# Optimization experiments

Hardware: AMD Instinct MI355X
Metric: run time of the kernel (lower is better)

Reference implementation:

```python
import jax, jax.numpy as jnp
import numpy as np

N, K, D_IN, H = 8192, 8, 512, 512
SCALE = 0.02  # weight init scale


def setup_inputs() -> dict:
    key = jax.random.key(0)
    ks = jax.random.split(key, 12)
    inp = {
        "x": jax.random.normal(ks[0], (N, D_IN), jnp.float32),
        "child_h": jax.random.normal(ks[1], (N, K, H), jnp.float32),
        "child_c": jax.random.normal(ks[2], (N, K, H), jnp.float32),
    }
    names = ["i", "f", "o", "u"]
    for idx, g in enumerate(names):
        inp["W" + g] = jax.random.normal(ks[3 + idx], (D_IN, H), jnp.float32) * SCALE
        inp["bW" + g] = jnp.zeros((H,), jnp.float32)
        inp["U" + g] = jax.random.normal(ks[7 + idx], (H, H), jnp.float32) * SCALE
        inp["bU" + g] = jnp.zeros((H,), jnp.float32)
    return inp


def reference(x, child_h, child_c,
              Wi, bWi, Ui, bUi,
              Wf, bWf, Uf, bUf,
              Wo, bWo, Uo, bUo,
              Wu, bWu, Uu, bUu):
    # Child-Sum Tree-LSTM, batched over N nodes each with K children.
    h_sum = child_h.sum(axis=1)                                   # [N, H]
    i = jax.nn.sigmoid(x @ Wi + bWi + h_sum @ Ui + bUi)           # [N, H]
    o = jax.nn.sigmoid(x @ Wo + bWo + h_sum @ Uo + bUo)           # [N, H]
    u = jnp.tanh(x @ Wu + bWu + h_sum @ Uu + bUu)                 # [N, H]
    # Per-child forget gates: f_k = sigmoid(W_f x + U_f h_k)
    f = jax.nn.sigmoid((x @ Wf + bWf)[:, None, :]
                       + jnp.einsum('nkh,hg->nkg', child_h, Uf) + bUf)  # [N, K, H]
    c = i * u + (f * child_c).sum(axis=1)                         # [N, H]
    h = o * jnp.tanh(c)                                           # [N, H]
    return jnp.stack([h, c], axis=0)                              # [2, N, H]
```

## Files before the change

kernel.cpp:

```cpp
#include <hip/hip_runtime.h>
#include <hip/hip_bf16.h>


#define NN 8192
#define KCH 8
#define HH 512

typedef __attribute__((ext_vector_type(4))) float f32x4;
typedef __attribute__((ext_vector_type(8))) short short8;

__device__ inline unsigned short f2bf(float f) {
    union { float f; unsigned u; } v; v.f = f;
    unsigned r = v.u + 0x7FFFu + ((v.u >> 16) & 1u);
    return (unsigned short)(r >> 16);
}
__device__ inline float bf2f(unsigned short b) {
    union { unsigned u; float f; } v; v.u = ((unsigned)b) << 16;
    return v.f;
}
__device__ inline float sigm(float x) { return 1.f / (1.f + __expf(-x)); }
__device__ inline float tanh_pf(float x) { return 2.f / (1.f + __expf(-2.f * x)) - 1.f; }

__device__ __forceinline__ void gl16(const unsigned short* gsrc, unsigned short* ldst) {
    __builtin_amdgcn_global_load_lds(
        (const __attribute__((address_space(1))) unsigned int*)gsrc,
        (__attribute__((address_space(3))) unsigned int*)ldst,
        16, 0, 0);
}


__global__ void k_cvt(const float* __restrict__ in, unsigned short* __restrict__ outp) {
    int i = blockIdx.x * blockDim.x + threadIdx.x;
    float4 a = ((const float4*)in)[2 * i];
    float4 b = ((const float4*)in)[2 * i + 1];
    uint4 o;
    o.x = (unsigned)f2bf(a.x) | ((unsigned)f2bf(a.y) << 16);
    o.y = (unsigned)f2bf(a.z) | ((unsigned)f2bf(a.w) << 16);
    o.z = (unsigned)f2bf(b.x) | ((unsigned)f2bf(b.y) << 16);
    o.w = (unsigned)f2bf(b.z) | ((unsigned)f2bf(b.w) << 16);
    ((uint4*)outp)[i] = o;
}

__global__ void k_hsum(const float* __restrict__ ch, unsigned short* __restrict__ hs) {
    int i = blockIdx.x * blockDim.x + threadIdx.x;
    int n = i >> 7, h4 = i & 127;
    const float4* base = (const float4*)(ch + (size_t)n * KCH * HH) + h4;
    float4 s = base[0];
#pragma unroll
    for (int k = 1; k < KCH; ++k) {
        float4 v = base[(size_t)k * 128];
        s.x += v.x; s.y += v.y; s.z += v.z; s.w += v.w;
    }
    unsigned long long pk = (unsigned long long)f2bf(s.x)
        | ((unsigned long long)f2bf(s.y) << 16)
        | ((unsigned long long)f2bf(s.z) << 32)
        | ((unsigned long long)f2bf(s.w) << 48);
    *(unsigned long long*)&hs[(size_t)i * 4] = pk;
}

struct P8 { const float* p[8]; };
__global__ void k_transpose_w(P8 wsrc, unsigned short* __restrict__ out) {
    __shared__ float tile[32][33];
    const float* W = wsrc.p[blockIdx.z];
    unsigned short* O = out + (size_t)blockIdx.z * 262144;
    int k0 = blockIdx.x * 32, c0 = blockIdx.y * 32;
    for (int r = threadIdx.y; r < 32; r += 8)
        tile[r][threadIdx.x] = W[(size_t)(k0 + r) * 512 + c0 + threadIdx.x];
    __syncthreads();
    for (int r = threadIdx.y; r < 32; r += 8)
        O[(size_t)(c0 + r) * 512 + k0 + threadIdx.x] = f2bf(tile[threadIdx.x][r]);
}

__device__ __forceinline__ void gate_mfma(f32x4 (&acc)[4][2], const short8 (&af)[4],
                                          const unsigned short (*bl)[32], int bcol, int koff) {
    short8 b0 = *(const short8*)&bl[bcol][koff];
    short8 b1 = *(const short8*)&bl[bcol + 16][koff];
#pragma unroll
    for (int m = 0; m < 4; ++m) {
        acc[m][0] = __builtin_amdgcn_mfma_f32_16x16x32_bf16(af[m], b0, acc[m][0], 0, 0, 0);
        acc[m][1] = __builtin_amdgcn_mfma_f32_16x16x32_bf16(af[m], b1, acc[m][1], 0, 0, 0);
    }
}

__global__ __launch_bounds__(256) void k_gates(
    const unsigned short* __restrict__ xb,
    const unsigned short* __restrict__ hsb,
    const unsigned short* __restrict__ wT,
    const float* __restrict__ bWi, const float* __restrict__ bUi,
    const float* __restrict__ bWf,
    const float* __restrict__ bWo, const float* __restrict__ bUo,
    const float* __restrict__ bWu, const float* __restrict__ bUu,
    unsigned short* __restrict__ Pq,
    unsigned short* __restrict__ Oq,
    unsigned short* __restrict__ Fq)
{
    __shared__ unsigned short a_lds[128][32];
    __shared__ unsigned short b_lds[4][64][32];
    const int t = threadIdx.x, lane = t & 63, wid = t >> 6;
    const int wr = wid >> 1, wc = wid & 1;
    const int nid = (blockIdx.x & 7) * 64 + (blockIdx.x >> 3);
    const int r0 = (nid >> 3) * 128, c0 = (nid & 7) * 64;

    f32x4 acc_i[4][2] = {}; f32x4 acc_f[4][2] = {};
    f32x4 acc_o[4][2] = {}; f32x4 acc_u[4][2] = {};

    const int koff = (lane >> 4) * 8;
    const int arow = wr * 64 + (lane & 15);
    const int bcol = wc * 32 + (lane & 15);
    const int rsub = lane >> 2, c8 = (lane & 3) * 8;

#pragma unroll 1
    for (int kq = 0; kq < 512; kq += 32) {
        __syncthreads();
        for (int c = wid; c < 24; c += 4) {
            if (c < 8) {
                gl16(&xb[(size_t)(r0 + c * 16 + rsub) * 512 + kq + c8], &a_lds[c * 16][0]);
            } else {
                int d = c - 8, p = d >> 2, cb = d & 3;
                gl16(&wT[(size_t)p * 262144 + (size_t)(c0 + cb * 16 + rsub) * 512 + kq + c8],
                     &b_lds[p][cb * 16][0]);
            }
        }
        __syncthreads();
        short8 af[4];
#pragma unroll
        for (int m = 0; m < 4; ++m) af[m] = *(const short8*)&a_lds[arow + m * 16][koff];
        gate_mfma(acc_i, af, b_lds[0], bcol, koff);
        gate_mfma(acc_f, af, b_lds[1], bcol, koff);
        gate_mfma(acc_o, af, b_lds[2], bcol, koff);
        gate_mfma(acc_u, af, b_lds[3], bcol, koff);
    }
#pragma unroll 1
    for (int kq = 0; kq < 512; kq += 32) {
        __syncthreads();
        for (int c = wid; c < 20; c += 4) {
            if (c < 8) {
                gl16(&hsb[(size_t)(r0 + c * 16 + rsub) * 512 + kq + c8], &a_lds[c * 16][0]);
            } else {
                int d = c - 8, p = d >> 2, cb = d & 3;
                gl16(&wT[(size_t)(4 + p) * 262144 + (size_t)(c0 + cb * 16 + rsub) * 512 + kq + c8],
                     &b_lds[p][cb * 16][0]);
            }
        }
        __syncthreads();
        short8 af[4];
#pragma unroll
        for (int m = 0; m < 4; ++m) af[m] = *(const short8*)&a_lds[arow + m * 16][koff];
        gate_mfma(acc_i, af, b_lds[0], bcol, koff);
        gate_mfma(acc_o, af, b_lds[1], bcol, koff);
        gate_mfma(acc_u, af, b_lds[2], bcol, koff);
    }
#pragma unroll
    for (int m = 0; m < 4; ++m) {
#pragma unroll
        for (int n = 0; n < 2; ++n) {
            int col = c0 + wc * 32 + n * 16 + (lane & 15);
            float bi = bWi[col] + bUi[col];
            float bf = bWf[col];
            float bo = bWo[col] + bUo[col];
            float bu = bWu[col] + bUu[col];
#pragma unroll
            for (int r = 0; r < 4; ++r) {
                int row = r0 + wr * 64 + m * 16 + (lane >> 4) * 4 + r;
                size_t idx = (size_t)row * 512 + col;
                float vi = sigm(acc_i[m][n][r] + bi);
                float vu = tanh_pf(acc_u[m][n][r] + bu);
                Pq[idx] = f2bf(vi * vu);
                Oq[idx] = f2bf(sigm(acc_o[m][n][r] + bo));
                Fq[idx] = f2bf(acc_f[m][n][r] + bf);
            }
        }
    }
}

__global__ __launch_bounds__(512, 2) void k_fc(
    const float* __restrict__ ch,
    const float* __restrict__ cc,
    const unsigned short* __restrict__ ufT,
    const float* __restrict__ bUf,
    const unsigned short* __restrict__ Pq,
    const unsigned short* __restrict__ Oq,
    const unsigned short* __restrict__ Fq,
    float* __restrict__ out)
{
    __shared__ unsigned short a_lds[64][32];
    __shared__ unsigned short b_lds[512][32];
    const int t = threadIdx.x, lane = t & 63, wid = t >> 6;
    const int wc = wid;
    const int r0c = blockIdx.x * 64;

    f32x4 acc[4][4] = {};
    const int koff = (lane >> 4) * 8;
    const int rsub = lane >> 2, cb8 = (lane & 3) * 8;
    const int sarow = t >> 3, sac4 = (t & 7) * 4;

#pragma unroll 1
    for (int kq = 0; kq < 512; kq += 32) {
        __syncthreads();
        {
            float4 v = *(const float4*)&ch[(size_t)(r0c + sarow) * 512 + kq + sac4];
            unsigned long long pk = (unsigned long long)f2bf(v.x)
                | ((unsigned long long)f2bf(v.y) << 16)
                | ((unsigned long long)f2bf(v.z) << 32)
                | ((unsigned long long)f2bf(v.w) << 48);
            *(unsigned long long*)&a_lds[sarow][sac4] = pk;
        }
        for (int c = wid; c < 32; c += 8)
            gl16(&ufT[(size_t)(c * 16 + rsub) * 512 + kq + cb8], &b_lds[c * 16][0]);
        __syncthreads();
        short8 af[4], bfr[4];
#pragma unroll
        for (int m = 0; m < 4; ++m) af[m] = *(const short8*)&a_lds[m * 16 + (lane & 15)][koff];
#pragma unroll
        for (int n = 0; n < 4; ++n) bfr[n] = *(const short8*)&b_lds[wc * 64 + n * 16 + (lane & 15)][koff];
#pragma unroll
        for (int m = 0; m < 4; ++m)
#pragma unroll
            for (int n = 0; n < 4; ++n)
                acc[m][n] = __builtin_amdgcn_mfma_f32_16x16x32_bf16(af[m], bfr[n], acc[m][n], 0, 0, 0);
    }

    const int g = lane >> 4;
    float bUfv[4];
#pragma unroll
    for (int n = 0; n < 4; ++n) bUfv[n] = bUf[wc * 64 + n * 16 + (lane & 15)];

#pragma unroll
    for (int m = 0; m < 4; ++m) {
        int node = (r0c >> 3) + 2 * m + (g >> 1);
#pragma unroll
        for (int n = 0; n < 4; ++n) {
            int col = wc * 64 + n * 16 + (lane & 15);
            size_t nidx = (size_t)node * 512 + col;
            float xf = bf2f(Fq[nidx]) + bUfv[n];
            float fcs = 0.f;
#pragma unroll
            for (int r = 0; r < 4; ++r) {
                int R = r0c + m * 16 + g * 4 + r;
                float pre = acc[m][n][r] + xf;
                fcs += sigm(pre) * cc[(size_t)R * 512 + col];
            }
            fcs += __shfl_xor(fcs, 16);
            if ((g & 1) == 0) {
                float cv = bf2f(Pq[nidx]) + fcs;
                out[nidx] = bf2f(Oq[nidx]) * tanh_pf(cv);
                out[(size_t)NN * HH + nidx] = cv;
            }
        }
    }
}

extern "C" void kernel_launch(void* const* d_in, const int* in_sizes, int n_in,
                              void* d_out, int out_size, void* d_ws, size_t ws_size,
                              hipStream_t stream) {
    const float* x   = (const float*)d_in[0];
    const float* ch  = (const float*)d_in[1];
    const float* cc  = (const float*)d_in[2];
    const float* Wi  = (const float*)d_in[3];  const float* bWi = (const float*)d_in[4];
    const float* Ui  = (const float*)d_in[5];  const float* bUi = (const float*)d_in[6];
    const float* Wf  = (const float*)d_in[7];  const float* bWf = (const float*)d_in[8];
    const float* Uf  = (const float*)d_in[9];  const float* bUf = (const float*)d_in[10];
    const float* Wo  = (const float*)d_in[11]; const float* bWo = (const float*)d_in[12];
    const float* Uo  = (const float*)d_in[13]; const float* bUo = (const float*)d_in[14];
    const float* Wu  = (const float*)d_in[15]; const float* bWu = (const float*)d_in[16];
    const float* Uu  = (const float*)d_in[17]; const float* bUu = (const float*)d_in[18];
    float* out = (float*)d_out;

    unsigned short* xb  = (unsigned short*)d_ws;
    unsigned short* hsb = xb  + (size_t)NN * HH;
    unsigned short* wT  = hsb + (size_t)NN * HH;
    unsigned short* Pq  = wT  + (size_t)8 * 262144;
    unsigned short* Oq  = Pq  + (size_t)NN * HH;
    unsigned short* Fq  = Oq  + (size_t)NN * HH;

    k_cvt<<<(NN * HH / 8) / 256, 256, 0, stream>>>(x, xb);
    k_hsum<<<(NN * 128) / 256, 256, 0, stream>>>(ch, hsb);
    P8 wp;
    wp.p[0] = Wi; wp.p[1] = Wf; wp.p[2] = Wo; wp.p[3] = Wu;
    wp.p[4] = Ui; wp.p[5] = Uo; wp.p[6] = Uu; wp.p[7] = Uf;
    k_transpose_w<<<dim3(16, 16, 8), dim3(32, 8), 0, stream>>>(wp, wT);
    k_gates<<<dim3(512), 256, 0, stream>>>(xb, hsb, wT,
                                           bWi, bUi, bWf, bWo, bUo, bWu, bUu,
                                           Pq, Oq, Fq);
    k_fc<<<dim3(1024), 512, 0, stream>>>(ch, cc, wT + (size_t)7 * 262144, bUf,
                                         Pq, Oq, Fq, out);
}
```

Measured before the change: 216.0 us.

## Double-buffer LDS staging in gate and forget-cell GEMM kernels

Both GEMM kernels now keep two LDS buffers. The next K-slice is staged into one buffer while MFMAs consume the other, which cuts each loop iteration to a single barrier and lets global loads overlap compute. The LDS layout also changes to fragment order (16x32 tiles stored contiguously by lane), so fragment reads become linear and avoid bank conflicts. The cost is more LDS per block (48KB and 72KB), which can limit occupancy, and the new launch_bounds(256,2) on k_gates constrains its register budget.

```diff
diff --git a/kernel.cpp b/kernel.cpp
--- a/kernel.cpp
+++ b/kernel.cpp
@@ -71,18 +71,7 @@
         O[(size_t)(c0 + r) * 512 + k0 + threadIdx.x] = f2bf(tile[threadIdx.x][r]);
 }
 
-__device__ __forceinline__ void gate_mfma(f32x4 (&acc)[4][2], const short8 (&af)[4],
-                                          const unsigned short (*bl)[32], int bcol, int koff) {
-    short8 b0 = *(const short8*)&bl[bcol][koff];
-    short8 b1 = *(const short8*)&bl[bcol + 16][koff];
-#pragma unroll
-    for (int m = 0; m < 4; ++m) {
-        acc[m][0] = __builtin_amdgcn_mfma_f32_16x16x32_bf16(af[m], b0, acc[m][0], 0, 0, 0);
-        acc[m][1] = __builtin_amdgcn_mfma_f32_16x16x32_bf16(af[m], b1, acc[m][1], 0, 0, 0);
-    }
-}
-
-__global__ __launch_bounds__(256) void k_gates(
+__global__ __launch_bounds__(256, 2) void k_gates(
     const unsigned short* __restrict__ xb,
     const unsigned short* __restrict__ hsb,
     const unsigned short* __restrict__ wT,
@@ -94,8 +83,7 @@
     unsigned short* __restrict__ Oq,
     unsigned short* __restrict__ Fq)
 {
-    __shared__ unsigned short a_lds[128][32];
-    __shared__ unsigned short b_lds[4][64][32];
+    __shared__ unsigned short lds[2][12288];
     const int t = threadIdx.x, lane = t & 63, wid = t >> 6;
     const int wr = wid >> 1, wc = wid & 1;
     const int nid = (blockIdx.x & 7) * 64 + (blockIdx.x >> 3);
@@ -104,51 +92,91 @@
     f32x4 acc_i[4][2] = {}; f32x4 acc_f[4][2] = {};
     f32x4 acc_o[4][2] = {}; f32x4 acc_u[4][2] = {};
 
-    const int koff = (lane >> 4) * 8;
-    const int arow = wr * 64 + (lane & 15);
-    const int bcol = wc * 32 + (lane & 15);
-    const int rsub = lane >> 2, c8 = (lane & 3) * 8;
+    const int frow = lane & 15, fk = (lane >> 4) * 8;
+
+    auto stage0 = [&](unsigned short* buf, int kq) {
+        for (int c = wid; c < 24; c += 4) {
+            if (c < 8) {
+                gl16(&xb[(size_t)(r0 + c * 16 + frow) * 512 + kq + fk], &buf[c * 512]);
+            } else {
+                int d = c - 8, p = d >> 2, cb = d & 3;
+                gl16(&wT[(size_t)p * 262144 + (size_t)(c0 + cb * 16 + frow) * 512 + kq + fk],
+                     &buf[4096 + d * 512]);
+            }
+        }
+    };
+    auto stage1 = [&](unsigned short* buf, int kq) {
+        for (int c = wid; c < 20; c += 4) {
+            if (c < 8) {
+                gl16(&hsb[(size_t)(r0 + c * 16 + frow) * 512 + kq + fk], &buf[c * 512]);
+            } else {
+                int d = c - 8, p = d >> 2, cb = d & 3;
+                gl16(&wT[(size_t)(4 + p) * 262144 + (size_t)(c0 + cb * 16 + frow) * 512 + kq + fk],
+                     &buf[4096 + d * 512]);
+            }
+        }
+    };
+
+    stage0(lds[0], 0);
 
 #pragma unroll 1
     for (int kq = 0; kq < 512; kq += 32) {
+        unsigned short* cur = lds[(kq >> 5) & 1];
+        unsigned short* nxt = lds[((kq >> 5) & 1) ^ 1];
         __syncthreads();
-        for (int c = wid; c < 24; c += 4) {
-            if (c < 8) {
-                gl16(&xb[(size_t)(r0 + c * 16 + rsub) * 512 + kq + c8], &a_lds[c * 16][0]);
-            } else {
-                int d = c - 8, p = d >> 2, cb = d & 3;
-                gl16(&wT[(size_t)p * 262144 + (size_t)(c0 + cb * 16 + rsub) * 512 + kq + c8],
-                     &b_lds[p][cb * 16][0]);
-            }
-        }
-        __syncthreads();
+        if (kq < 480) stage0(nxt, kq + 32); else stage1(nxt, 0);
         short8 af[4];
 #pragma unroll
-        for (int m = 0; m < 4; ++m) af[m] = *(const short8*)&a_lds[arow + m * 16][koff];
-        gate_mfma(acc_i, af, b_lds[0], bcol, koff);
-        gate_mfma(acc_f, af, b_lds[1], bcol, koff);
-        gate_mfma(acc_o, af, b_lds[2], bcol, koff);
-        gate_mfma(acc_u, af, b_lds[3], bcol, koff);
+        for (int m = 0; m < 4; ++m) af[m] = *(const short8*)&cur[(wr * 4 + m) * 512 + lane * 8];
+#pragma unroll
+        for (int p = 0; p < 4; ++p) {
+            short8 b0 = *(const short8*)&cur[4096 + (p * 4 + wc * 2 + 0) * 512 + lane * 8];
+            short8 b1 = *(const short8*)&cur[4096 + (p * 4 + wc * 2 + 1) * 512 + lane * 8];
+#pragma unroll
+            for (int m = 0; m < 4; ++m) {
+                if (p == 0) {
+                    acc_i[m][0] = __builtin_amdgcn_mfma_f32_16x16x32_bf16(af[m], b0, acc_i[m][0], 0, 0, 0);
+                    acc_i[m][1] = __builtin_amdgcn_mfma_f32_16x16x32_bf16(af[m], b1, acc_i[m][1], 0, 0, 0);
+                } else if (p == 1) {
+                    acc_f[m][0] = __builtin_amdgcn_mfma_f32_16x16x32_bf16(af[m], b0, acc_f[m][0], 0, 0, 0);
+                    acc_f[m][1] = __builtin_amdgcn_mfma_f32_16x16x32_bf16(af[m], b1, acc_f[m][1], 0, 0, 0);
+                } else if (p == 2) {
+                    acc_o[m][0] = __builtin_amdgcn_mfma_f32_16x16x32_bf16(af[m], b0, acc_o[m][0], 0, 0, 0);
+                    acc_o[m][1] = __builtin_amdgcn_mfma_f32_16x16x32_bf16(af[m], b1, acc_o[m][1], 0, 0, 0);
+                } else {
+                    acc_u[m][0] = __builtin_amdgcn_mfma_f32_16x16x32_bf16(af[m], b0, acc_u[m][0], 0, 0, 0);
+                    acc_u[m][1] = __builtin_amdgcn_mfma_f32_16x16x32_bf16(af[m], b1, acc_u[m][1], 0, 0, 0);
+                }
+            }
+        }
     }
 #pragma unroll 1
     for (int kq = 0; kq < 512; kq += 32) {
+        unsigned short* cur = lds[(kq >> 5) & 1];
+        unsigned short* nxt = lds[((kq >> 5) & 1) ^ 1];
         __syncthreads();
-        for (int c = wid; c < 20; c += 4) {
-            if (c < 8) {
-                gl16(&hsb[(size_t)(r0 + c * 16 + rsub) * 512 + kq + c8], &a_lds[c * 16][0]);
-            } else {
-                int d = c - 8, p = d >> 2, cb = d & 3;
-                gl16(&wT[(size_t)(4 + p) * 262144 + (size_t)(c0 + cb * 16 + rsub) * 512 + kq + c8],
-                     &b_lds[p][cb * 16][0]);
-            }
-        }
-        __syncthreads();
+        if (kq < 480) stage1(nxt, kq + 32);
         short8 af[4];
 #pragma unroll
-        for (int m = 0; m < 4; ++m) af[m] = *(const short8*)&a_lds[arow + m * 16][koff];
-        gate_mfma(acc_i, af, b_lds[0], bcol, koff);
-        gate_mfma(acc_o, af, b_lds[1], bcol, koff);
-        gate_mfma(acc_u, af, b_lds[2], bcol, koff);
+        for (int m = 0; m < 4; ++m) af[m] = *(const short8*)&cur[(wr * 4 + m) * 512 + lane * 8];
+#pragma unroll
+        for (int p = 0; p < 3; ++p) {
+            short8 b0 = *(const short8*)&cur[4096 + (p * 4 + wc * 2 + 0) * 512 + lane * 8];
+            short8 b1 = *(const short8*)&cur[4096 + (p * 4 + wc * 2 + 1) * 512 + lane * 8];
+#pragma unroll
+            for (int m = 0; m < 4; ++m) {
+                if (p == 0) {
+                    acc_i[m][0] = __builtin_amdgcn_mfma_f32_16x16x32_bf16(af[m], b0, acc_i[m][0], 0, 0, 0);
+                    acc_i[m][1] = __builtin_amdgcn_mfma_f32_16x16x32_bf16(af[m], b1, acc_i[m][1], 0, 0, 0);
+                } else if (p == 1) {
+                    acc_o[m][0] = __builtin_amdgcn_mfma_f32_16x16x32_bf16(af[m], b0, acc_o[m][0], 0, 0, 0);
+                    acc_o[m][1] = __builtin_amdgcn_mfma_f32_16x16x32_bf16(af[m], b1, acc_o[m][1], 0, 0, 0);
+                } else {
+                    acc_u[m][0] = __builtin_amdgcn_mfma_f32_16x16x32_bf16(af[m], b0, acc_u[m][0], 0, 0, 0);
+                    acc_u[m][1] = __builtin_amdgcn_mfma_f32_16x16x32_bf16(af[m], b1, acc_u[m][1], 0, 0, 0);
+                }
+            }
+        }
     }
 #pragma unroll
     for (int m = 0; m < 4; ++m) {
@@ -183,36 +211,49 @@
     const unsigned short* __restrict__ Fq,
     float* __restrict__ out)
 {
-    __shared__ unsigned short a_lds[64][32];
-    __shared__ unsigned short b_lds[512][32];
+    __shared__ unsigned short lds[2][18432];
     const int t = threadIdx.x, lane = t & 63, wid = t >> 6;
     const int wc = wid;
     const int r0c = blockIdx.x * 64;
 
     f32x4 acc[4][4] = {};
-    const int koff = (lane >> 4) * 8;
-    const int rsub = lane >> 2, cb8 = (lane & 3) * 8;
-    const int sarow = t >> 3, sac4 = (t & 7) * 4;
+    const int frow = lane & 15, fk = (lane >> 4) * 8;
+
+    auto stage = [&](unsigned short* buf, int kq) {
+        if (t < 256) {
+            int row = 16 * (t >> 6) + (t & 15), ks = (t >> 4) & 3;
+            const float* src = &ch[(size_t)(r0c + row) * 512 + kq + ks * 8];
+            float4 v0 = *(const float4*)src;
+            float4 v1 = *(const float4*)(src + 4);
+            uint4 o;
+            o.x = (unsigned)f2bf(v0.x) | ((unsigned)f2bf(v0.y) << 16);
+            o.y = (unsigned)f2bf(v0.z) | ((unsigned)f2bf(v0.w) << 16);
+            o.z = (unsigned)f2bf(v1.x) | ((unsigned)f2bf(v1.y) << 16);
+            o.w = (unsigned)f2bf(v1.z) | ((unsigned)f2bf(v1.w) << 16);
+            *(uint4*)&buf[t * 8] = o;
+        } else {
+            int w = wid - 4;
+#pragma unroll
+            for (int j = 0; j < 8; ++j) {
+                int s2 = w * 8 + j;
+                gl16(&ufT[(size_t)(s2 * 16 + frow) * 512 + kq + fk], &buf[2048 + s2 * 512]);
+            }
+        }
+    };
+
+    stage(lds[0], 0);
 
 #pragma unroll 1
     for (int kq = 0; kq < 512; kq += 32) {
+        unsigned short* cur = lds[(kq >> 5) & 1];
+        unsigned short* nxt = lds[((kq >> 5) & 1) ^ 1];
         __syncthreads();
-        {
-            float4 v = *(const float4*)&ch[(size_t)(r0c + sarow) * 512 + kq + sac4];
-            unsigned long long pk = (unsigned long long)f2bf(v.x)
-                | ((unsigned long long)f2bf(v.y) << 16)
-                | ((unsigned long long)f2bf(v.z) << 32)
-                | ((unsigned long long)f2bf(v.w) << 48);
-            *(unsigned long long*)&a_lds[sarow][sac4] = pk;
-        }
-        for (int c = wid; c < 32; c += 8)
-            gl16(&ufT[(size_t)(c * 16 + rsub) * 512 + kq + cb8], &b_lds[c * 16][0]);
-        __syncthreads();
+        if (kq < 480) stage(nxt, kq + 32);
         short8 af[4], bfr[4];
 #pragma unroll
-        for (int m = 0; m < 4; ++m) af[m] = *(const short8*)&a_lds[m * 16 + (lane & 15)][koff];
-#pragma unroll
-        for (int n = 0; n < 4; ++n) bfr[n] = *(const short8*)&b_lds[wc * 64 + n * 16 + (lane & 15)][koff];
+        for (int m = 0; m < 4; ++m) af[m] = *(const short8*)&cur[m * 512 + lane * 8];
+#pragma unroll
+        for (int n = 0; n < 4; ++n) bfr[n] = *(const short8*)&cur[2048 + (wc * 4 + n) * 512 + lane * 8];
 #pragma unroll
         for (int m = 0; m < 4; ++m)
 #pragma unroll
```

Measured after the change: 212.0 us. No clear change (-1.9%).
